# Optimization experiments

Hardware: AMD Instinct MI355X
Metric: run time of the kernel (lower is better)

The kernel has to match this reference:

```python
import jax, jax.numpy as jnp
import numpy as np

DIM = 1024
HEADS = 16
DIM_HEAD = 64
INNER = HEADS * DIM_HEAD
SCALE = DIM_HEAD ** -0.5


def rotate_half(t):
    # '... (j d) -> ... j d' with j=2: split last dim in half
    x1, x2 = jnp.split(t, 2, axis=-1)
    return jnp.concatenate((-x2, x1), axis=-1)


def rotary_pos(n, d, dtype):
    inv_freq = 1.0 / (10000.0 ** (jnp.arange(0, d, 2, dtype=jnp.float32) / d))
    freqs = jnp.arange(n, dtype=jnp.float32)[:, None] * inv_freq[None, :]  # (n, d/2)
    return jnp.concatenate((freqs, freqs), axis=-1).astype(dtype)  # (n, d)


def apply_rope(pos, t):
    return t * jnp.cos(pos) + rotate_half(t) * jnp.sin(pos)


def setup_inputs() -> dict:
    key = jax.random.key(0)
    ks = jax.random.split(key, 5)
    x = jax.random.normal(ks[0], (2, 2048, DIM), dtype=jnp.float32)
    gamma = jnp.ones((DIM,), dtype=jnp.float32)
    beta = jnp.zeros((DIM,), dtype=jnp.float32)
    Wq = jax.random.normal(ks[1], (DIM, INNER), dtype=jnp.float32) * 0.02
    Wkv = jax.random.normal(ks[2], (DIM, 2 * INNER), dtype=jnp.float32) * 0.02
    Wo = jax.random.normal(ks[3], (INNER, DIM), dtype=jnp.float32) * 0.02
    return {"x": x, "gamma": gamma, "beta": beta, "Wq": Wq, "Wkv": Wkv, "Wo": Wo}


def reference(x, gamma, beta, Wq, Wkv, Wo):
    b, n, _ = x.shape
    # LayerNorm with learned gamma, fixed-zero beta buffer
    mu = jnp.mean(x, axis=-1, keepdims=True)
    var = jnp.var(x, axis=-1, keepdims=True)
    xn = (x - mu) / jnp.sqrt(var + 1e-5) * gamma + beta

    q = xn @ Wq                       # (b, n, inner)
    kv = xn @ Wkv
    k, v = jnp.split(kv, 2, axis=-1)

    def to_heads(t):
        return t.reshape(b, n, HEADS, DIM_HEAD).transpose(0, 2, 1, 3)  # b h n d

    q, k, v = map(to_heads, (q, k, v))

    pos = rotary_pos(n, DIM_HEAD, x.dtype)  # (n, d)
    q = apply_rope(pos, q)
    k = apply_rope(pos, k)

    q = q * SCALE
    sim = jnp.einsum('bhid,bhjd->bhij', q, k)

    neg = -jnp.finfo(sim.dtype).max
    causal_mask = jnp.triu(jnp.ones((n, n), dtype=bool), k=1)
    sim = jnp.where(causal_mask, neg, sim)

    attn = jax.nn.softmax(sim, axis=-1)
    out = jnp.einsum('bhij,bhjd->bhid', attn, v)
    out = out.transpose(0, 2, 1, 3).reshape(b, n, INNER)
    return out @ Wo
```

## Files before the change

### kernel.cpp

```cpp
#include <hip/hip_runtime.h>
#include <stdint.h>

typedef unsigned short u16;
typedef __attribute__((ext_vector_type(8))) short short8;
typedef __attribute__((ext_vector_type(4))) float floatx4;
typedef __attribute__((ext_vector_type(4))) unsigned short u16x4;
typedef __attribute__((ext_vector_type(2))) unsigned int uint2v;

__device__ __forceinline__ float bf2f(u16 v) {
  union { uint32_t u; float f; } x; x.u = ((uint32_t)v) << 16; return x.f;
}
__device__ __forceinline__ u16 f2bf(float f) {
  union { float f; uint32_t u; } x; x.f = f;
  uint32_t r = x.u + 0x7fffu + ((x.u >> 16) & 1u);
  return (u16)(r >> 16);
}
__device__ __forceinline__ uint32_t fu(float f) {
  union { float f; uint32_t u; } x; x.f = f; return x.u;
}

#define GL2LDS(g, l)                                                          \
  __builtin_amdgcn_global_load_lds(                                           \
      (const __attribute__((address_space(1))) void*)(g),                     \
      (__attribute__((address_space(3))) void*)(l), 16, 0, 0)

__global__ __launch_bounds__(256) void prep_k(const float* __restrict__ x,
                                              const float* __restrict__ gamma,
                                              const float* __restrict__ beta,
                                              const float* __restrict__ Wq,
                                              const float* __restrict__ Wkv,
                                              const float* __restrict__ Wo,
                                              u16* __restrict__ xn,
                                              u16* __restrict__ wqkvT,
                                              u16* __restrict__ woT) {
  int bid = blockIdx.x;
  int t = threadIdx.x;
  if (bid < 4096) {
    int row = bid;
    const float* xr = x + (size_t)row * 1024;
    float4 xv = *(const float4*)(xr + t * 4);
    float v0 = xv.x, v1 = xv.y, v2 = xv.z, v3 = xv.w;
    float s = v0 + v1 + v2 + v3;
    float s2 = v0 * v0 + v1 * v1 + v2 * v2 + v3 * v3;
#pragma unroll
    for (int d = 1; d < 64; d <<= 1) {
      s += __shfl_xor(s, d, 64);
      s2 += __shfl_xor(s2, d, 64);
    }
    __shared__ float red[8];
    int lane = t & 63, wv = t >> 6;
    if (lane == 0) { red[wv] = s; red[4 + wv] = s2; }
    __syncthreads();
    s = red[0] + red[1] + red[2] + red[3];
    s2 = red[4] + red[5] + red[6] + red[7];
    float mu = s * (1.0f / 1024.0f);
    float var = s2 * (1.0f / 1024.0f) - mu * mu;
    float rstd = rsqrtf(var + 1e-5f);
    float4 gv = *(const float4*)(gamma + t * 4);
    float4 bv = *(const float4*)(beta + t * 4);
    u16x4 ov;
    ov.x = f2bf((v0 - mu) * rstd * gv.x + bv.x);
    ov.y = f2bf((v1 - mu) * rstd * gv.y + bv.y);
    ov.z = f2bf((v2 - mu) * rstd * gv.z + bv.z);
    ov.w = f2bf((v3 - mu) * rstd * gv.w + bv.w);
    *(u16x4*)(xn + (size_t)row * 1024 + t * 4) = ov;
  } else {
    __shared__ float tile[32][33];
    int wb = bid - 4096;
    const float* in;
    u16* outp;
    int C;
    if (wb < 1024) { in = Wq; outp = wqkvT; C = 1024; }
    else if (wb < 3072) { wb -= 1024; in = Wkv; outp = wqkvT + 1024 * 1024; C = 2048; }
    else { wb -= 3072; in = Wo; outp = woT; C = 1024; }
    int nbx = C >> 5;
    int c0 = (wb % nbx) * 32, r0 = (wb / nbx) * 32;
    int tx = t & 31, ty = t >> 5;
#pragma unroll
    for (int i = 0; i < 32; i += 8)
      tile[ty + i][tx] = in[(size_t)(r0 + ty + i) * C + c0 + tx];
    __syncthreads();
#pragma unroll
    for (int i = 0; i < 32; i += 8)
      outp[(size_t)(c0 + ty + i) * 1024 + r0 + tx] = f2bf(tile[tx][ty + i]);
  }
}

__global__ __launch_bounds__(256) void gemm_qkv_k(const u16* __restrict__ A,
                                                  const u16* __restrict__ BT,
                                                  u16* __restrict__ C) {
  const int K = 1024, lda = 1024, ldc = 3072;
  __shared__ __align__(16) u16 lA[128 * 32];
  __shared__ __align__(16) u16 lB[128 * 32];
  int tid = threadIdx.x;
  int bm = blockIdx.y * 128;
  int bn = blockIdx.x * 128;
  int w = tid >> 6, l = tid & 63;
  int wm = (w >> 1) * 64, wn = (w & 1) * 64;
  int lr = l & 15, lq = l >> 4;
  floatx4 acc[4][4] = {};
  int sr = w * 16 + (l >> 2);
  int sc = (l & 3) * 8;
  for (int k0 = 0; k0 < K; k0 += 32) {
    GL2LDS(A + (size_t)(bm + sr) * lda + k0 + sc, &lA[sr * 32 + sc]);
    GL2LDS(A + (size_t)(bm + sr + 64) * lda + k0 + sc, &lA[(sr + 64) * 32 + sc]);
    GL2LDS(BT + (size_t)(bn + sr) * K + k0 + sc, &lB[sr * 32 + sc]);
    GL2LDS(BT + (size_t)(bn + sr + 64) * K + k0 + sc, &lB[(sr + 64) * 32 + sc]);
    __syncthreads();
    short8 afr[4], bfr[4];
#pragma unroll
    for (int i = 0; i < 4; i++)
      afr[i] = *(const short8*)(&lA[(wm + i * 16 + lr) * 32 + lq * 8]);
#pragma unroll
    for (int i = 0; i < 4; i++)
      bfr[i] = *(const short8*)(&lB[(wn + i * 16 + lr) * 32 + lq * 8]);
#pragma unroll
    for (int mi = 0; mi < 4; mi++)
#pragma unroll
      for (int ni = 0; ni < 4; ni++)
        acc[mi][ni] = __builtin_amdgcn_mfma_f32_16x16x32_bf16(
            afr[mi], bfr[ni], acc[mi][ni], 0, 0, 0);
    __syncthreads();
  }
  int sec = bn >> 10;
  if (sec == 2) {
#pragma unroll
    for (int mi = 0; mi < 4; mi++)
#pragma unroll
      for (int ni = 0; ni < 4; ni++)
#pragma unroll
        for (int r = 0; r < 4; r++) {
          int row = bm + wm + mi * 16 + lq * 4 + r;
          int col = bn + wn + ni * 16 + lr;
          C[(size_t)row * ldc + col] = f2bf(acc[mi][ni][r]);
        }
  } else {
    float QS = (sec == 0) ? 0.125f * 1.44269504088896f : 1.0f;
#pragma unroll
    for (int ni = 0; ni < 2; ni++) {
      int i = ni * 16 + lr;
      float invf = exp2f(-(float)i * 0.4152410118609203f);
#pragma unroll
      for (int mi = 0; mi < 4; mi++)
#pragma unroll
        for (int r = 0; r < 4; r++) {
          int row = bm + wm + mi * 16 + lq * 4 + r;
          int n = row & 2047;
          float ang = (float)n * invf;
          float s_, c_;
          __sincosf(ang, &s_, &c_);
          float x1 = acc[mi][ni][r], x2 = acc[mi][ni + 2][r];
          int col = bn + wn + ni * 16 + lr;
          C[(size_t)row * ldc + col] = f2bf((x1 * c_ - x2 * s_) * QS);
          C[(size_t)row * ldc + col + 32] = f2bf((x2 * c_ + x1 * s_) * QS);
        }
    }
  }
}

__global__ __launch_bounds__(256) void gemm64_bf16_k(const u16* __restrict__ A,
                                                     const u16* __restrict__ BT,
                                                     float* __restrict__ C,
                                                     int K, int lda, int ldc) {
  __shared__ __align__(16) u16 lA[64 * 32];
  __shared__ __align__(16) u16 lB[128 * 32];
  int tid = threadIdx.x;
  int bm = blockIdx.y * 64;
  int bn = blockIdx.x * 128;
  int w = tid >> 6, l = tid & 63;
  int wm = (w >> 1) * 32, wn = (w & 1) * 64;
  int lr = l & 15, lq = l >> 4;
  floatx4 acc[2][4] = {};
  int sr = w * 16 + (l >> 2);
  int sc = (l & 3) * 8;
  for (int k0 = 0; k0 < K; k0 += 32) {
    GL2LDS(A + (size_t)(bm + sr) * lda + k0 + sc, &lA[sr * 32 + sc]);
    GL2LDS(BT + (size_t)(bn + sr) * K + k0 + sc, &lB[sr * 32 + sc]);
    GL2LDS(BT + (size_t)(bn + sr + 64) * K + k0 + sc, &lB[(sr + 64) * 32 + sc]);
    __syncthreads();
    short8 afr[2], bfr[4];
#pragma unroll
    for (int i = 0; i < 2; i++)
      afr[i] = *(const short8*)(&lA[(wm + i * 16 + lr) * 32 + lq * 8]);
#pragma unroll
    for (int i = 0; i < 4; i++)
      bfr[i] = *(const short8*)(&lB[(wn + i * 16 + lr) * 32 + lq * 8]);
#pragma unroll
    for (int mi = 0; mi < 2; mi++)
#pragma unroll
      for (int ni = 0; ni < 4; ni++)
        acc[mi][ni] = __builtin_amdgcn_mfma_f32_16x16x32_bf16(
            afr[mi], bfr[ni], acc[mi][ni], 0, 0, 0);
    __syncthreads();
  }
#pragma unroll
  for (int mi = 0; mi < 2; mi++)
#pragma unroll
    for (int ni = 0; ni < 4; ni++)
#pragma unroll
      for (int r = 0; r < 4; r++) {
        int row = bm + wm + mi * 16 + lq * 4 + r;
        int col = bn + wn + ni * 16 + lr;
        C[(size_t)row * ldc + col] = acc[mi][ni][r];
      }
}

__global__ __launch_bounds__(256) void vt_k(const u16* __restrict__ qkv,
                                            u16* __restrict__ vT) {
  __shared__ u16 tile[32][33];
  int vb = blockIdx.x;
  int bh = vb >> 7;
  int rest = vb & 127;
  int d0 = (rest >> 6) * 32;
  int n0 = (rest & 63) * 32;
  int b = bh >> 4, h = bh & 15;
  int tid = threadIdx.x;
  int tx = tid & 31, ty = tid >> 5;
#pragma unroll
  for (int i = 0; i < 32; i += 8)
    tile[ty + i][tx] =
        qkv[(size_t)(b * 2048 + n0 + ty + i) * 3072 + 2048 + h * 64 + d0 + tx];
  __syncthreads();
#pragma unroll
  for (int i = 0; i < 32; i += 8)
    vT[((size_t)bh * 64 + d0 + ty + i) * 2048 + n0 + tx] = tile[tx][ty + i];
}

#define LPT 72
__device__ __forceinline__ void attn_tile2(const u16* lK, const u16* lV, u16* lp,
                                           const short8* aq, floatx4* o,
                                           float& m_i, float& l_i, int lr, int lq,
                                           bool diag, int q0, int k0g,
                                           short8 ones) {
  floatx4 s[4];
#pragma unroll
  for (int ni = 0; ni < 4; ni++) {
    floatx4 a = {};
#pragma unroll
    for (int kc = 0; kc < 2; kc++) {
      int R = ni * 16 + lr;
      int c8 = (kc * 4 + lq) ^ (R & 7);
      short8 kf = *(const short8*)&lK[R * 64 + c8 * 8];
      a = __builtin_amdgcn_mfma_f32_16x16x32_bf16(kf, aq[kc], a, 0, 0, 0);
    }
    s[ni] = a;
  }
  if (diag) {
    int qg = q0 + lr;
#pragma unroll
    for (int ni = 0; ni < 4; ni++)
#pragma unroll
      for (int r = 0; r < 4; r++) {
        int kg = k0g + ni * 16 + lq * 4 + r;
        if (kg > qg) s[ni][r] = -1e30f;
      }
  }
  float mx = fmaxf(fmaxf(s[0][0], s[0][1]), fmaxf(s[0][2], s[0][3]));
#pragma unroll
  for (int ni = 1; ni < 4; ni++)
    mx = fmaxf(mx, fmaxf(fmaxf(s[ni][0], s[ni][1]), fmaxf(s[ni][2], s[ni][3])));
  mx = fmaxf(mx, __shfl_xor(mx, 16, 64));
  mx = fmaxf(mx, __shfl_xor(mx, 32, 64));
  float mnew = fmaxf(m_i, mx);
  float alpha = exp2f(m_i - mnew);
  m_i = mnew;
#pragma unroll
  for (int ni = 0; ni < 4; ni++) {
    float p0 = exp2f(s[ni][0] - mnew), p1 = exp2f(s[ni][1] - mnew);
    float p2 = exp2f(s[ni][2] - mnew), p3 = exp2f(s[ni][3] - mnew);
    uint2v dw;
    dw.x = __builtin_amdgcn_perm(fu(p1), fu(p0), 0x07060302u);
    dw.y = __builtin_amdgcn_perm(fu(p3), fu(p2), 0x07060302u);
    *(uint2v*)&lp[lr * LPT + ni * 16 + lq * 4] = dw;
  }
  short8 pb0 = *(const short8*)&lp[lr * LPT + lq * 8];
  short8 pb1 = *(const short8*)&lp[lr * LPT + 32 + lq * 8];
  floatx4 z = {};
  z = __builtin_amdgcn_mfma_f32_16x16x32_bf16(ones, pb0, z, 0, 0, 0);
  z = __builtin_amdgcn_mfma_f32_16x16x32_bf16(ones, pb1, z, 0, 0, 0);
  l_i = l_i * alpha + z[0];
#pragma unroll
  for (int di = 0; di < 4; di++)
#pragma unroll
    for (int r = 0; r < 4; r++) o[di][r] *= alpha;
#pragma unroll
  for (int di = 0; di < 4; di++) {
    int R = di * 16 + lr;
    int c80 = lq ^ (R & 7);
    int c81 = (4 + lq) ^ (R & 7);
    short8 v0 = *(const short8*)&lV[R * 64 + c80 * 8];
    o[di] = __builtin_amdgcn_mfma_f32_16x16x32_bf16(v0, pb0, o[di], 0, 0, 0);
    short8 v1 = *(const short8*)&lV[R * 64 + c81 * 8];
    o[di] = __builtin_amdgcn_mfma_f32_16x16x32_bf16(v1, pb1, o[di], 0, 0, 0);
  }
}

__global__ __launch_bounds__(256) void attn_k(const u16* __restrict__ qkv,
                                              const u16* __restrict__ vt,
                                              u16* __restrict__ out) {
  __shared__ __align__(16) u16 lK[2][64 * 64];
  __shared__ __align__(16) u16 lV[2][64 * 64];
  __shared__ __align__(16) u16 lP[4][16 * LPT];
  int bh = blockIdx.y;
  int b = bh >> 4, h = bh & 15;
  int p = blockIdx.x;
  int jB = 31 - p;
  int tid = threadIdx.x;
  int w = tid >> 6, l = tid & 63;
  int lr = l & 15, lq = l >> 4;
  int q0A = p * 64 + w * 16;
  int q0B = jB * 64 + w * 16;
  const u16* qb = qkv + (size_t)b * 2048 * 3072 + h * 64;
  const u16* kb = qkv + (size_t)b * 2048 * 3072 + 1024 + h * 64;
  const u16* vb = vt + (size_t)bh * 64 * 2048;
  short8 aqA[2], aqB[2];
  aqA[0] = *(const short8*)(qb + (size_t)(q0A + lr) * 3072 + lq * 8);
  aqA[1] = *(const short8*)(qb + (size_t)(q0A + lr) * 3072 + 32 + lq * 8);
  aqB[0] = *(const short8*)(qb + (size_t)(q0B + lr) * 3072 + lq * 8);
  aqB[1] = *(const short8*)(qb + (size_t)(q0B + lr) * 3072 + 32 + lq * 8);
  short8 ones;
#pragma unroll
  for (int i = 0; i < 8; i++) ones[i] = (short)0x3F80;
  floatx4 oA[4] = {}, oB[4] = {};
  float mA = -1e30f, lA_ = 0.0f, mB = -1e30f, lB_ = 0.0f;
  int srow8 = l >> 3;
  int sc8 = (l & 7) ^ srow8;
  u16* lp = &lP[w][0];
  auto stage = [&](int bufi, int kt) {
#pragma unroll
    for (int c = 0; c < 2; c++) {
      int m = w + c * 4;
      int row = m * 8 + srow8;
      GL2LDS(kb + (size_t)(kt * 64 + row) * 3072 + sc8 * 8, &lK[bufi][m * 512]);
      GL2LDS(vb + (size_t)row * 2048 + kt * 64 + sc8 * 8, &lV[bufi][m * 512]);
    }
  };
  stage(0, 0);
  for (int kt = 0; kt <= jB; ++kt) {
    int cur = kt & 1;
    __syncthreads();
    if (kt < jB) stage(cur ^ 1, kt + 1);
    attn_tile2(lK[cur], lV[cur], lp, aqB, oB, mB, lB_, lr, lq, kt == jB, q0B,
               kt * 64, ones);
    if (kt <= p)
      attn_tile2(lK[cur], lV[cur], lp, aqA, oA, mA, lA_, lr, lq, kt == p, q0A,
                 kt * 64, ones);
  }
  float rlA = 1.0f / lA_, rlB = 1.0f / lB_;
#pragma unroll
  for (int di = 0; di < 4; di++) {
    uint2v dwA, dwB;
    u16 a0 = f2bf(oA[di][0] * rlA), a1 = f2bf(oA[di][1] * rlA);
    u16 a2 = f2bf(oA[di][2] * rlA), a3 = f2bf(oA[di][3] * rlA);
    dwA.x = (uint32_t)a0 | ((uint32_t)a1 << 16);
    dwA.y = (uint32_t)a2 | ((uint32_t)a3 << 16);
    u16 b0 = f2bf(oB[di][0] * rlB), b1 = f2bf(oB[di][1] * rlB);
    u16 b2 = f2bf(oB[di][2] * rlB), b3 = f2bf(oB[di][3] * rlB);
    dwB.x = (uint32_t)b0 | ((uint32_t)b1 << 16);
    dwB.y = (uint32_t)b2 | ((uint32_t)b3 << 16);
    int dcol = h * 64 + di * 16 + lq * 4;
    *(uint2v*)(out + ((size_t)(b * 2048 + q0A + lr)) * 3072 + dcol) = dwA;
    *(uint2v*)(out + ((size_t)(b * 2048 + q0B + lr)) * 3072 + dcol) = dwB;
  }
}

extern "C" void kernel_launch(void* const* d_in, const int* in_sizes, int n_in,
                              void* d_out, int out_size, void* d_ws, size_t ws_size,
                              hipStream_t stream) {
  const float* x = (const float*)d_in[0];
  const float* gamma = (const float*)d_in[1];
  const float* beta = (const float*)d_in[2];
  const float* Wq = (const float*)d_in[3];
  const float* Wkv = (const float*)d_in[4];
  const float* Wo = (const float*)d_in[5];
  float* out = (float*)d_out;
  char* ws = (char*)d_ws;

  u16* qkv = (u16*)(ws);
  u16* wqkvT = (u16*)(ws + 25165824);
  u16* woT = (u16*)(ws + 31457280);
  u16* xn = (u16*)(ws + 33554432);
  u16* vT = xn;
  u16* attn_out = qkv + 2048;

  prep_k<<<8192, 256, 0, stream>>>(x, gamma, beta, Wq, Wkv, Wo, xn, wqkvT, woT);
  gemm_qkv_k<<<dim3(24, 32), 256, 0, stream>>>(xn, wqkvT, qkv);
  vt_k<<<4096, 256, 0, stream>>>(qkv, vT);
  attn_k<<<dim3(16, 32), 256, 0, stream>>>(qkv, vT, attn_out);
  gemm64_bf16_k<<<dim3(8, 64), 256, 0, stream>>>(attn_out, woT, out, 1024, 3072, 1024);
}
```

Baseline: 216.2 us.

## Fuse V transpose into QKV GEMM, split-K output GEMM, skip unneeded rescale

The QKV GEMM epilogue now writes V directly in transposed per-head layout, which removes the separate transpose kernel and its extra read/write pass. The output projection uses a two-way split-K with atomic float adds, and prep_k gets extra blocks that zero the output first, to raise parallelism. The attention inner loop skips the alpha rescale of the accumulator when no lane's running max changed. Risks include scattered strided stores in the epilogue, atomic contention and extra output zeroing traffic, and a nondeterministic summation order.

```diff
diff --git a/kernel.cpp b/kernel.cpp
--- a/kernel.cpp
+++ b/kernel.cpp
@@ -32,7 +32,8 @@
                                               const float* __restrict__ Wo,
                                               u16* __restrict__ xn,
                                               u16* __restrict__ wqkvT,
-                                              u16* __restrict__ woT) {
+                                              u16* __restrict__ woT,
+                                              float* __restrict__ outz) {
   int bid = blockIdx.x;
   int t = threadIdx.x;
   if (bid < 4096) {
@@ -64,7 +65,7 @@
     ov.z = f2bf((v2 - mu) * rstd * gv.z + bv.z);
     ov.w = f2bf((v3 - mu) * rstd * gv.w + bv.w);
     *(u16x4*)(xn + (size_t)row * 1024 + t * 4) = ov;
-  } else {
+  } else if (bid < 8192) {
     __shared__ float tile[32][33];
     int wb = bid - 4096;
     const float* in;
@@ -83,12 +84,17 @@
 #pragma unroll
     for (int i = 0; i < 32; i += 8)
       outp[(size_t)(c0 + ty + i) * 1024 + r0 + tx] = f2bf(tile[tx][ty + i]);
+  } else {
+    size_t idx = ((size_t)(bid - 8192) * 256 + t) * 4;
+    float4 z = {0.0f, 0.0f, 0.0f, 0.0f};
+    *(float4*)(outz + idx) = z;
   }
 }
 
 __global__ __launch_bounds__(256) void gemm_qkv_k(const u16* __restrict__ A,
                                                   const u16* __restrict__ BT,
-                                                  u16* __restrict__ C) {
+                                                  u16* __restrict__ C,
+                                                  u16* __restrict__ vT) {
   const int K = 1024, lda = 1024, ldc = 3072;
   __shared__ __align__(16) u16 lA[128 * 32];
   __shared__ __align__(16) u16 lB[128 * 32];
@@ -125,15 +131,22 @@
   int sec = bn >> 10;
   if (sec == 2) {
 #pragma unroll
-    for (int mi = 0; mi < 4; mi++)
-#pragma unroll
-      for (int ni = 0; ni < 4; ni++)
-#pragma unroll
-        for (int r = 0; r < 4; r++) {
-          int row = bm + wm + mi * 16 + lq * 4 + r;
-          int col = bn + wn + ni * 16 + lr;
-          C[(size_t)row * ldc + col] = f2bf(acc[mi][ni][r]);
-        }
+    for (int ni = 0; ni < 4; ni++) {
+      int dg = bn - 2048 + wn + ni * 16 + lr;
+      int h = dg >> 6, d = dg & 63;
+#pragma unroll
+      for (int mi = 0; mi < 4; mi++) {
+        int row = bm + wm + mi * 16 + lq * 4;
+        int b = row >> 11, n = row & 2047;
+        int bh = b * 16 + h;
+        uint2v dw;
+        u16 a0 = f2bf(acc[mi][ni][0]), a1 = f2bf(acc[mi][ni][1]);
+        u16 a2 = f2bf(acc[mi][ni][2]), a3 = f2bf(acc[mi][ni][3]);
+        dw.x = (uint32_t)a0 | ((uint32_t)a1 << 16);
+        dw.y = (uint32_t)a2 | ((uint32_t)a3 << 16);
+        *(uint2v*)(vT + ((size_t)bh * 64 + d) * 2048 + n) = dw;
+      }
+    }
   } else {
     float QS = (sec == 0) ? 0.125f * 1.44269504088896f : 1.0f;
 #pragma unroll
@@ -158,22 +171,24 @@
   }
 }
 
-__global__ __launch_bounds__(256) void gemm64_bf16_k(const u16* __restrict__ A,
-                                                     const u16* __restrict__ BT,
-                                                     float* __restrict__ C,
-                                                     int K, int lda, int ldc) {
+__global__ __launch_bounds__(256) void gemm64sk_k(const u16* __restrict__ A,
+                                                  const u16* __restrict__ BT,
+                                                  float* __restrict__ C,
+                                                  int K, int lda, int ldc) {
   __shared__ __align__(16) u16 lA[64 * 32];
   __shared__ __align__(16) u16 lB[128 * 32];
   int tid = threadIdx.x;
   int bm = blockIdx.y * 64;
   int bn = blockIdx.x * 128;
+  int kh = K >> 1;
+  int kbeg = blockIdx.z * kh, kend = kbeg + kh;
   int w = tid >> 6, l = tid & 63;
   int wm = (w >> 1) * 32, wn = (w & 1) * 64;
   int lr = l & 15, lq = l >> 4;
   floatx4 acc[2][4] = {};
   int sr = w * 16 + (l >> 2);
   int sc = (l & 3) * 8;
-  for (int k0 = 0; k0 < K; k0 += 32) {
+  for (int k0 = kbeg; k0 < kend; k0 += 32) {
     GL2LDS(A + (size_t)(bm + sr) * lda + k0 + sc, &lA[sr * 32 + sc]);
     GL2LDS(BT + (size_t)(bn + sr) * K + k0 + sc, &lB[sr * 32 + sc]);
     GL2LDS(BT + (size_t)(bn + sr + 64) * K + k0 + sc, &lB[(sr + 64) * 32 + sc]);
@@ -201,29 +216,8 @@
       for (int r = 0; r < 4; r++) {
         int row = bm + wm + mi * 16 + lq * 4 + r;
         int col = bn + wn + ni * 16 + lr;
-        C[(size_t)row * ldc + col] = acc[mi][ni][r];
+        unsafeAtomicAdd(&C[(size_t)row * ldc + col], acc[mi][ni][r]);
       }
-}
-
-__global__ __launch_bounds__(256) void vt_k(const u16* __restrict__ qkv,
-                                            u16* __restrict__ vT) {
-  __shared__ u16 tile[32][33];
-  int vb = blockIdx.x;
-  int bh = vb >> 7;
-  int rest = vb & 127;
-  int d0 = (rest >> 6) * 32;
-  int n0 = (rest & 63) * 32;
-  int b = bh >> 4, h = bh & 15;
-  int tid = threadIdx.x;
-  int tx = tid & 31, ty = tid >> 5;
-#pragma unroll
-  for (int i = 0; i < 32; i += 8)
-    tile[ty + i][tx] =
-        qkv[(size_t)(b * 2048 + n0 + ty + i) * 3072 + 2048 + h * 64 + d0 + tx];
-  __syncthreads();
-#pragma unroll
-  for (int i = 0; i < 32; i += 8)
-    vT[((size_t)bh * 64 + d0 + ty + i) * 2048 + n0 + tx] = tile[tx][ty + i];
 }
 
 #define LPT 72
@@ -262,6 +256,7 @@
   mx = fmaxf(mx, __shfl_xor(mx, 16, 64));
   mx = fmaxf(mx, __shfl_xor(mx, 32, 64));
   float mnew = fmaxf(m_i, mx);
+  bool nochg = (mnew == m_i);
   float alpha = exp2f(m_i - mnew);
   m_i = mnew;
 #pragma unroll
@@ -278,11 +273,15 @@
   floatx4 z = {};
   z = __builtin_amdgcn_mfma_f32_16x16x32_bf16(ones, pb0, z, 0, 0, 0);
   z = __builtin_amdgcn_mfma_f32_16x16x32_bf16(ones, pb1, z, 0, 0, 0);
-  l_i = l_i * alpha + z[0];
-#pragma unroll
-  for (int di = 0; di < 4; di++)
-#pragma unroll
-    for (int r = 0; r < 4; r++) o[di][r] *= alpha;
+  if (__ballot(nochg) != ~0ULL) {
+    l_i = l_i * alpha + z[0];
+#pragma unroll
+    for (int di = 0; di < 4; di++)
+#pragma unroll
+      for (int r = 0; r < 4; r++) o[di][r] *= alpha;
+  } else {
+    l_i += z[0];
+  }
 #pragma unroll
   for (int di = 0; di < 4; di++) {
     int R = di * 16 + lr;
@@ -383,9 +382,12 @@
   u16* vT = xn;
   u16* attn_out = qkv + 2048;
 
-  prep_k<<<8192, 256, 0, stream>>>(x, gamma, beta, Wq, Wkv, Wo, xn, wqkvT, woT);
-  gemm_qkv_k<<<dim3(24, 32), 256, 0, stream>>>(xn, wqkvT, qkv);
-  vt_k<<<4096, 256, 0, stream>>>(qkv, vT);
+  vT = (u16*)(ws + 41943040);
+
+  prep_k<<<12288, 256, 0, stream>>>(x, gamma, beta, Wq, Wkv, Wo, xn, wqkvT, woT,
+                                    out);
+  gemm_qkv_k<<<dim3(24, 32), 256, 0, stream>>>(xn, wqkvT, qkv, vT);
   attn_k<<<dim3(16, 32), 256, 0, stream>>>(qkv, vT, attn_out);
-  gemm64_bf16_k<<<dim3(8, 64), 256, 0, stream>>>(attn_out, woT, out, 1024, 3072, 1024);
-}
+  gemm64sk_k<<<dim3(8, 64, 2), 256, 0, stream>>>(attn_out, woT, out, 1024, 3072,
+                                                 1024);
+}
```

After: 232.2 us. 7.4% more time.
